# Performance work log

Hardware: AMD Instinct MI355X
Metric: run time of the kernel (lower is better)

## Reference

```python
import jax, jax.numpy as jnp
import numpy as np

S, B, D, L = 100, 2048, 128, 2  # seq_len, batch, dim_model, n_layers
LN_EPS = 1e-5


def _layer_norm(x, g, b):
    # x: [S, B, D]; normalize over last dim (nn.LayerNorm(dim))
    mu = jnp.mean(x, axis=-1, keepdims=True)
    var = jnp.mean(jnp.square(x - mu), axis=-1, keepdims=True)
    return (x - mu) * jax.lax.rsqrt(var + LN_EPS) * g + b


def _asb(x, cw, cwh, thr):
    # Adaptive_Spectral_Block. x: [S, B, D] -> permute to [B, N, C]
    xb = jnp.transpose(x, (1, 0, 2)).astype(jnp.float32)  # [B, N, C]
    N = xb.shape[1]
    x_fft = jnp.fft.rfft(xb, axis=1, norm='ortho')  # [B, F, C] complex, F = N//2+1
    w = jax.lax.complex(cw[:, 0], cw[:, 1])          # [C]
    x_weighted = x_fft * w
    # adaptive high-frequency mask
    energy = jnp.sum(jnp.square(jnp.abs(x_fft)), axis=-1)  # [B, F]
    F = energy.shape[1]
    # torch.median returns the LOWER of the two middle values -> k-th smallest, k=(F-1)//2
    median = jnp.sort(energy, axis=1)[:, (F - 1) // 2][:, None]  # [B, 1]
    norm_e = energy / (median + 1e-6)
    threshold = jnp.quantile(norm_e, thr)  # global scalar quantile (linear interp, as torch)
    mask = (norm_e < threshold)[..., None].astype(x_fft.real.dtype)  # [B, F, 1]
    wh = jax.lax.complex(cwh[:, 0], cwh[:, 1])       # [C]
    x_weighted = x_weighted + (x_fft * mask) * wh
    out = jnp.fft.irfft(x_weighted, n=N, axis=1, norm='ortho')  # [B, N, C]
    return jnp.transpose(out, (1, 0, 2)).astype(x.dtype)  # back to [S, B, D]


def setup_inputs() -> dict:
    key = jax.random.key(0)
    k0, k1, k2, k3 = jax.random.split(key, 4)
    return {
        'x': jax.random.normal(k0, (S, B, D), dtype=jnp.float32),
        'complex_weight': jax.random.normal(k1, (L, D, 2), dtype=jnp.float32) * 0.02,
        'complex_weight_high': jax.random.normal(k2, (L, D, 2), dtype=jnp.float32) * 0.02,
        'threshold_param': jax.random.uniform(k3, (L,), dtype=jnp.float32) * 0.5,
        'gamma': jnp.ones((L, D), dtype=jnp.float32),
        'beta': jnp.zeros((L, D), dtype=jnp.float32),
    }


def reference(x, complex_weight, complex_weight_high, threshold_param, gamma, beta):
    # Encoder.forward: nlayers x (x = x + ASB(LayerNorm(x)))
    for i in range(L):
        h = _layer_norm(x, gamma[i], beta[i])
        x = x + _asb(h, complex_weight[i], complex_weight_high[i], threshold_param[i])
    return x
```

## Files before the change

kernel.cpp:

```cpp
#include <hip/hip_runtime.h>
#include <math.h>

#define SEQ    100
#define BATCH  2048
#define DIM    128
#define NF     51
#define NLAYER 2
#define MTOT   (BATCH * NF)
#define BD     (BATCH * DIM)

typedef __attribute__((ext_vector_type(8))) short bf16x8;
typedef __attribute__((ext_vector_type(4))) float f32x4v;

__device__ __forceinline__ unsigned short f2bf(float f) {
    unsigned u = __float_as_uint(f);
    return (unsigned short)((u + 0x7FFFu + ((u >> 16) & 1u)) >> 16);
}

__global__ void k_tables(unsigned short* __restrict__ imgF,
                         unsigned short* __restrict__ imgI) {
    const int i = blockIdx.x * 256 + threadIdx.x;
    const float W = 6.28318530717958647692f / 100.f;
    if (i < 2 * 64 * 128) {
        const int p = i >> 13, k = (i >> 7) & 63, n = i & 127;
        float v = 0.f;
        if (k < NF && n < SEQ) {
            float s, c; sincosf((float)((k * n) % 100) * W, &s, &c);
            v = 0.1f * (p ? -s : c);
        }
        imgF[i] = f2bf(v);
    }
    if (i < 2 * 128 * 64) {
        const int p = i >> 13, n = (i >> 6) & 127, k = i & 63;
        float v = 0.f;
        if (k < NF && n < SEQ) {
            float s, c; sincosf((float)((k * n) % 100) * W, &s, &c);
            const float a = (k == 0 || k == 50) ? 0.1f : 0.2f;
            v = p ? -a * s : a * c;
        }
        imgI[i] = f2bf(v);
    }
}

__device__ __forceinline__ void ln_stage(const float* __restrict__ x,
                                         const float* __restrict__ gamma,
                                         const float* __restrict__ beta,
                                         unsigned short* hT, int b, int t)
{
    const int lane = t & 63, wv = t >> 6;
    const int c0 = lane * 2;
    const float2 gv = *(const float2*)&gamma[c0];
    const float2 bv = *(const float2*)&beta[c0];

    #pragma unroll
    for (int slot = 0; slot < 4; ++slot) {
        const int chunk = slot * 4 + wv;
        const int n0 = chunk * 8;
        float2 v[8];
        #pragma unroll
        for (int j = 0; j < 8; ++j)
            if (n0 + j < SEQ)
                v[j] = *(const float2*)&x[(size_t)(n0 + j) * BD + (size_t)b * DIM + c0];
        unsigned we[4], wo[4];
        #pragma unroll
        for (int j = 0; j < 8; ++j) {
            unsigned short he = 0, ho = 0;
            if (n0 + j < SEQ) {
                float s  = v[j].x + v[j].y;
                float s2 = fmaf(v[j].x, v[j].x, v[j].y * v[j].y);
                #pragma unroll
                for (int off = 1; off < 64; off <<= 1) {
                    s  += __shfl_xor(s,  off, 64);
                    s2 += __shfl_xor(s2, off, 64);
                }
                const float mu   = s * (1.f / 128.f);
                const float rstd = rsqrtf(s2 * (1.f / 128.f) - mu * mu + 1e-5f);
                he = f2bf(fmaf((v[j].x - mu) * rstd, gv.x, bv.x));
                ho = f2bf(fmaf((v[j].y - mu) * rstd, gv.y, bv.y));
            }
            if (j & 1) { we[j >> 1] |= (unsigned)he << 16; wo[j >> 1] |= (unsigned)ho << 16; }
            else       { we[j >> 1]  = he;                 wo[j >> 1]  = ho; }
        }
        const int sw = (chunk ^ (lane & 7)) << 3;
        int4 ve; ve.x = (int)we[0]; ve.y = (int)we[1]; ve.z = (int)we[2]; ve.w = (int)we[3];
        int4 vo; vo.x = (int)wo[0]; vo.y = (int)wo[1]; vo.z = (int)wo[2]; vo.w = (int)wo[3];
        *(int4*)&hT[(c0    ) * 128 + sw] = ve;
        *(int4*)&hT[(c0 + 1) * 128 + sw] = vo;
    }
}

__global__ __launch_bounds__(256, 4) void k_fwd(
    const float* __restrict__ x,
    const float* __restrict__ gamma, const float* __restrict__ beta,
    const unsigned short* __restrict__ imgF,
    float* __restrict__ normE)
{
    __shared__ __align__(16) unsigned short hT[128 * 128];
    __shared__ float epart[64][4];
    __shared__ float energy_s[64];
    __shared__ float med_s;

    const int b = blockIdx.x, t = threadIdx.x;
    const int lane = t & 63, wv = t >> 6, g4 = lane >> 4, cc = lane & 15;

    ln_stage(x, gamma, beta, hT, b, t);
    __syncthreads();

    bf16x8 Bf[2][4];
    #pragma unroll
    for (int ct = 0; ct < 2; ++ct) {
        const int c = wv * 32 + ct * 16 + cc;
        #pragma unroll
        for (int ks = 0; ks < 4; ++ks)
            Bf[ct][ks] = *(const bf16x8*)&hT[c * 128 + (((ks * 4 + g4) ^ (cc >> 1)) << 3)];
    }

    #pragma unroll
    for (int mt = 0; mt < 4; ++mt) {
        const int kr = mt * 16 + cc;
        f32x4v aR[2], aI[2];
        aR[0] = aR[1] = aI[0] = aI[1] = (f32x4v){0.f, 0.f, 0.f, 0.f};
        #pragma unroll
        for (int ks = 0; ks < 4; ++ks) {
            const int e0 = kr * 128 + ks * 32 + g4 * 8;
            const bf16x8 A0 = *(const bf16x8*)&imgF[e0];
            const bf16x8 A1 = *(const bf16x8*)&imgF[8192 + e0];
            #pragma unroll
            for (int ct = 0; ct < 2; ++ct) {
                aR[ct] = __builtin_amdgcn_mfma_f32_16x16x32_bf16(A0, Bf[ct][ks], aR[ct], 0, 0, 0);
                aI[ct] = __builtin_amdgcn_mfma_f32_16x16x32_bf16(A1, Bf[ct][ks], aI[ct], 0, 0, 0);
            }
        }
        #pragma unroll
        for (int reg = 0; reg < 4; ++reg) {
            float e = aR[0][reg] * aR[0][reg] + aI[0][reg] * aI[0][reg]
                    + aR[1][reg] * aR[1][reg] + aI[1][reg] * aI[1][reg];
            e += __shfl_xor(e, 1, 64); e += __shfl_xor(e, 2, 64);
            e += __shfl_xor(e, 4, 64); e += __shfl_xor(e, 8, 64);
            if (cc == 0) epart[mt * 16 + g4 * 4 + reg][wv] = e;
        }
    }
    __syncthreads();
    if (t < 64) energy_s[t] = epart[t][0] + epart[t][1] + epart[t][2] + epart[t][3];
    __syncthreads();
    if (t < NF) {
        const float e = energy_s[t];
        int cnt = 0;
        for (int j = 0; j < NF; ++j) {
            const float ej = energy_s[j];
            cnt += (ej < e || (ej == e && j < t)) ? 1 : 0;
        }
        if (cnt == (NF - 1) / 2) med_s = e;
    }
    __syncthreads();
    if (t < NF) normE[b * NF + t] = energy_s[t] / (med_s + 1e-6f);
}

__global__ void k_hist0(const float* __restrict__ normE,
                        unsigned* __restrict__ hist)
{
    __shared__ unsigned lh[2048];
    for (int i = threadIdx.x; i < 2048; i += 256) lh[i] = 0;
    __syncthreads();
    for (int i = blockIdx.x * 256 + threadIdx.x; i < MTOT; i += gridDim.x * 256)
        atomicAdd(&lh[__float_as_uint(normE[i]) >> 21], 1u);
    __syncthreads();
    for (int i = threadIdx.x; i < 2048; i += 256) {
        const unsigned c = lh[i];
        if (c) atomicAdd(&hist[i], c);
    }
}

__global__ void k_sel(const float* __restrict__ normE,
                      unsigned* __restrict__ hist,
                      unsigned* __restrict__ sel,
                      unsigned* __restrict__ done,
                      const float* __restrict__ thrp,
                      const int layer, const int phase,
                      float* __restrict__ thresh)
{
    __shared__ unsigned lh[4096];
    __shared__ unsigned sp[2], sc[2];
    __shared__ unsigned ticket_s;
    __shared__ float vb[2];
    const int t = threadIdx.x;
    const float q = thrp[layer] * (float)(MTOT - 1);
    const unsigned r0 = (unsigned)floorf(q);

    if (phase == 1) {
        if (t < 128) {
            const int j = t >> 6, ln = t & 63;
            const unsigned rk = r0 + (unsigned)j;
            unsigned sum = 0;
            for (int i = 0; i < 32; ++i) sum += hist[ln * 32 + i];
            unsigned pre = sum;
            #pragma unroll
            for (int off = 1; off < 64; off <<= 1) {
                const unsigned tt = __shfl_up(pre, off, 64);
                if (ln >= off) pre += tt;
            }
            const unsigned excl = pre - sum;
            if (rk >= excl && rk < excl + sum) {
                unsigned cum = excl;
                for (int i = 0; i < 32; ++i) {
                    const unsigned hc = hist[ln * 32 + i];
                    if (rk < cum + hc) { sp[j] = (unsigned)(ln * 32 + i) << 21; sc[j] = cum; break; }
                    cum += hc;
                }
            }
        }
    } else {
        if (t < 2) { sp[t] = sel[2 * t]; sc[t] = sel[2 * t + 1]; }
    }
    __syncthreads();
    const unsigned p0 = sp[0], p1 = sp[1];
    const int bins      = (phase == 1) ? 2048 : 1024;
    const int shift     = (phase == 1) ? 10 : 0;
    const unsigned hmsk = (phase == 1) ? 0xFFE00000u : 0xFFFFFC00u;
    const int region    = (phase == 1) ? 2048 : 6144;

    for (int i = t; i < 2 * bins; i += 256) lh[i] = 0;
    __syncthreads();
    for (int i = blockIdx.x * 256 + t; i < MTOT; i += gridDim.x * 256) {
        const unsigned v = __float_as_uint(normE[i]);
        const unsigned bin = (v >> shift) & (unsigned)(bins - 1);
        if ((v & hmsk) == p0) atomicAdd(&lh[bin], 1u);
        if ((v & hmsk) == p1) atomicAdd(&lh[bins + bin], 1u);
    }
    __syncthreads();
    for (int i = t; i < 2 * bins; i += 256) {
        const unsigned c = lh[i];
        if (c) atomicAdd(&hist[region + i], c);
    }
    __threadfence();
    if (t == 0) ticket_s = atomicAdd(&done[(layer << 1) + (phase - 1)], 1u);
    __syncthreads();
    if (ticket_s != (unsigned)(gridDim.x - 1)) return;
    __threadfence();

    if (t < 128) {
        const int j = t >> 6, ln = t & 63;
        const unsigned rk  = r0 + (unsigned)j;
        const unsigned rem = rk - sc[j];
        const unsigned* H  = hist + region + j * bins;
        const int per = bins / 64;
        unsigned sum = 0;
        for (int i = 0; i < per; ++i)
            sum += __hip_atomic_load(&H[ln * per + i], __ATOMIC_RELAXED, __HIP_MEMORY_SCOPE_AGENT);
        unsigned pre = sum;
        #pragma unroll
        for (int off = 1; off < 64; off <<= 1) {
            const unsigned tt = __shfl_up(pre, off, 64);
            if (ln >= off) pre += tt;
        }
        const unsigned excl = pre - sum;
        if (rem >= excl && rem < excl + sum) {
            unsigned cum = excl;
            for (int i = 0; i < per; ++i) {
                const unsigned hc = __hip_atomic_load(&H[ln * per + i],
                                        __ATOMIC_RELAXED, __HIP_MEMORY_SCOPE_AGENT);
                if (rem < cum + hc) {
                    const unsigned bin = (unsigned)(ln * per + i);
                    if (phase == 1) { sel[2 * j] = sp[j] | (bin << 10); sel[2 * j + 1] = sc[j] + cum; }
                    else            vb[j] = __uint_as_float(sp[j] | bin);
                    break;
                }
                cum += hc;
            }
        }
    }
    __syncthreads();
    if (phase == 1) { for (int i = t; i < 6144; i += 256) hist[i] = 0u; }
    else            { for (int i = t; i < 2048; i += 256) hist[6144 + i] = 0u; }
    if (t == 0) {
        done[(layer << 1) + (phase - 1)] = 0u;
        if (phase == 2) {
            const float frac = q - floorf(q);
            thresh[0] = vb[0] * (1.f - frac) + vb[1] * frac;
        }
    }
}

__global__ __launch_bounds__(256, 4) void k_asb(
    const float* __restrict__ x,
    const float* __restrict__ gamma, const float* __restrict__ beta,
    const float* __restrict__ cw, const float* __restrict__ cwh,
    const unsigned short* __restrict__ imgF,
    const unsigned short* __restrict__ imgI,
    const float* __restrict__ normE, const float* __restrict__ thresh,
    float* __restrict__ out)
{
    __shared__ __align__(16) unsigned short hT[128 * 128];
    __shared__ float mask_s[64];

    const int b = blockIdx.x, t = threadIdx.x;
    const int lane = t & 63, wv = t >> 6, g4 = lane >> 4, cc = lane & 15;

    if (t < 64) mask_s[t] = (t < NF && normE[b * NF + t] < thresh[0]) ? 1.f : 0.f;
    ln_stage(x, gamma, beta, hT, b, t);
    __syncthreads();

    bf16x8 Bf[2][4];
    #pragma unroll
    for (int ct = 0; ct < 2; ++ct) {
        const int c = wv * 32 + ct * 16 + cc;
        #pragma unroll
        for (int ks = 0; ks < 4; ++ks)
            Bf[ct][ks] = *(const bf16x8*)&hT[c * 128 + (((ks * 4 + g4) ^ (cc >> 1)) << 3)];
    }

    float fwr[2], fwi[2], fhr[2], fhi[2];
    #pragma unroll
    for (int ct = 0; ct < 2; ++ct) {
        const int c = wv * 32 + ct * 16 + cc;
        const float2 w2 = *(const float2*)&cw[2 * c];
        const float2 h2 = *(const float2*)&cwh[2 * c];
        fwr[ct] = w2.x; fwi[ct] = w2.y; fhr[ct] = h2.x; fhi[ct] = h2.y;
    }

    #pragma unroll
    for (int mt = 0; mt < 4; ++mt) {
        const int kr = mt * 16 + cc;
        f32x4v aR[2], aI[2];
        aR[0] = aR[1] = aI[0] = aI[1] = (f32x4v){0.f, 0.f, 0.f, 0.f};
        #pragma unroll
        for (int ks = 0; ks < 4; ++ks) {
            const int e0 = kr * 128 + ks * 32 + g4 * 8;
            const bf16x8 A0 = *(const bf16x8*)&imgF[e0];
            const bf16x8 A1 = *(const bf16x8*)&imgF[8192 + e0];
            #pragma unroll
            for (int ct = 0; ct < 2; ++ct) {
                aR[ct] = __builtin_amdgcn_mfma_f32_16x16x32_bf16(A0, Bf[ct][ks], aR[ct], 0, 0, 0);
                aI[ct] = __builtin_amdgcn_mfma_f32_16x16x32_bf16(A1, Bf[ct][ks], aI[ct], 0, 0, 0);
            }
        }
        #pragma unroll
        for (int ct = 0; ct < 2; ++ct) {
            const int c = wv * 32 + ct * 16 + cc;
            unsigned wr[2], wi[2];
            #pragma unroll
            for (int reg = 0; reg < 4; ++reg) {
                const float m   = mask_s[mt * 16 + g4 * 4 + reg];
                const float fre = fmaf(m, fhr[ct], fwr[ct]);
                const float fim = fmaf(m, fhi[ct], fwi[ct]);
                const float xr = aR[ct][reg], xi = aI[ct][reg];
                const unsigned short yr = f2bf(xr * fre - xi * fim);
                const unsigned short yi = f2bf(xr * fim + xi * fre);
                if (reg & 1) { wr[reg >> 1] |= (unsigned)yr << 16; wi[reg >> 1] |= (unsigned)yi << 16; }
                else         { wr[reg >> 1]  = yr;                 wi[reg >> 1]  = yi; }
            }
            const int chY = mt * 2 + (g4 >> 1);
            const int eb  = c * 128 + ((chY ^ (cc >> 1)) << 3) + (g4 & 1) * 4;
            int2 vr; vr.x = (int)wr[0]; vr.y = (int)wr[1];
            int2 vi; vi.x = (int)wi[0]; vi.y = (int)wi[1];
            *(int2*)&hT[eb]      = vr;
            *(int2*)&hT[eb + 64] = vi;
        }
    }

    bf16x8 Yr[2][2], Yi[2][2];
    #pragma unroll
    for (int ct = 0; ct < 2; ++ct) {
        const int c = wv * 32 + ct * 16 + cc;
        #pragma unroll
        for (int kb = 0; kb < 2; ++kb) {
            const int sw = (((kb * 4 + g4) ^ (cc >> 1)) << 3);
            Yr[ct][kb] = *(const bf16x8*)&hT[c * 128 + sw];
            Yi[ct][kb] = *(const bf16x8*)&hT[c * 128 + 64 + sw];
        }
    }

    #pragma unroll
    for (int mt = 0; mt < 7; ++mt) {
        const int nr = mt * 16 + cc;
        f32x4v o[2];
        o[0] = o[1] = (f32x4v){0.f, 0.f, 0.f, 0.f};
        #pragma unroll
        for (int kb = 0; kb < 2; ++kb) {
            const int e0 = nr * 64 + kb * 32 + g4 * 8;
            const bf16x8 A0 = *(const bf16x8*)&imgI[e0];
            const bf16x8 A1 = *(const bf16x8*)&imgI[8192 + e0];
            #pragma unroll
            for (int ct = 0; ct < 2; ++ct) {
                o[ct] = __builtin_amdgcn_mfma_f32_16x16x32_bf16(A0, Yr[ct][kb], o[ct], 0, 0, 0);
                o[ct] = __builtin_amdgcn_mfma_f32_16x16x32_bf16(A1, Yi[ct][kb], o[ct], 0, 0, 0);
            }
        }
        #pragma unroll
        for (int ct = 0; ct < 2; ++ct) {
            const int c = wv * 32 + ct * 16 + cc;
            #pragma unroll
            for (int reg = 0; reg < 4; ++reg) {
                const int n = mt * 16 + g4 * 4 + reg;
                if (n < SEQ) {
                    const size_t idx = (size_t)n * BD + (size_t)b * DIM + c;
                    out[idx] = x[idx] + o[ct][reg];
                }
            }
        }
    }
}

extern "C" void kernel_launch(void* const* d_in, const int* in_sizes, int n_in,
                              void* d_out, int out_size, void* d_ws, size_t ws_size,
                              hipStream_t stream)
{
    (void)in_sizes; (void)n_in; (void)out_size; (void)ws_size;
    const float* x    = (const float*)d_in[0];
    const float* cw   = (const float*)d_in[1];
    const float* cwh  = (const float*)d_in[2];
    const float* thrp = (const float*)d_in[3];
    const float* gam  = (const float*)d_in[4];
    const float* bet  = (const float*)d_in[5];
    float* out = (float*)d_out;

    char* ws = (char*)d_ws;
    unsigned short* imgF = (unsigned short*)(ws);
    unsigned short* imgI = (unsigned short*)(ws + 32768);
    float* normE   = (float*)(ws + 65536);
    unsigned* hist = (unsigned*)(ws + 483328);
    unsigned* done = (unsigned*)(ws + 516096);
    unsigned* sel  = (unsigned*)(ws + 516160);
    float* thresh  = (float*)(ws + 516224);

    k_tables<<<64, 256, 0, stream>>>(imgF, imgI);
    hipMemsetAsync(hist, 0, 32768 + 64, stream);

    for (int l = 0; l < NLAYER; ++l) {
        const float* xi = (l == 0) ? x : out;
        k_fwd<<<BATCH, 256, 0, stream>>>(xi, gam + l * DIM, bet + l * DIM,
                                         imgF, normE);
        k_hist0<<<96, 256, 0, stream>>>(normE, hist);
        k_sel<<<96, 256, 0, stream>>>(normE, hist, sel, done, thrp, l, 1, thresh);
        k_sel<<<96, 256, 0, stream>>>(normE, hist, sel, done, thrp, l, 2, thresh);
        k_asb<<<BATCH, 256, 0, stream>>>(xi, gam + l * DIM, bet + l * DIM,
                                         cw + l * DIM * 2, cwh + l * DIM * 2,
                                         imgF, imgI, normE, thresh, out);
    }
}
```

Baseline: 423.7 us.

## Store forward spectrum in workspace and skip LayerNorm+DFT recompute in ASB kernel

k_fwd now writes the bf16 forward-DFT spectrum (real and imaginary, per batch and channel) into a 64 MB workspace buffer. k_asb reads that buffer and applies the weight and mask directly, so it no longer repeats the LayerNorm and forward DFT matmuls. The LN stage is also inlined, with all x loads issued before any reduction to raise memory-level parallelism. The trade is extra global write and read traffic of about 64 MB each per layer, and a larger workspace, in return for removing redundant compute and x reads in the second kernel.

```diff
diff --git a/kernel.cpp b/kernel.cpp
--- a/kernel.cpp
+++ b/kernel.cpp
@@ -8,6 +8,7 @@
 #define NLAYER 2
 #define MTOT   (BATCH * NF)
 #define BD     (BATCH * DIM)
+#define XSTR   16384
 
 typedef __attribute__((ext_vector_type(8))) short bf16x8;
 typedef __attribute__((ext_vector_type(4))) float f32x4v;
@@ -15,6 +16,9 @@
 __device__ __forceinline__ unsigned short f2bf(float f) {
     unsigned u = __float_as_uint(f);
     return (unsigned short)((u + 0x7FFFu + ((u >> 16) & 1u)) >> 16);
+}
+__device__ __forceinline__ float bf2f(unsigned short u) {
+    return __uint_as_float((unsigned)u << 16);
 }
 
 __global__ void k_tables(unsigned short* __restrict__ imgF,
@@ -42,57 +46,11 @@
     }
 }
 
-__device__ __forceinline__ void ln_stage(const float* __restrict__ x,
-                                         const float* __restrict__ gamma,
-                                         const float* __restrict__ beta,
-                                         unsigned short* hT, int b, int t)
-{
-    const int lane = t & 63, wv = t >> 6;
-    const int c0 = lane * 2;
-    const float2 gv = *(const float2*)&gamma[c0];
-    const float2 bv = *(const float2*)&beta[c0];
-
-    #pragma unroll
-    for (int slot = 0; slot < 4; ++slot) {
-        const int chunk = slot * 4 + wv;
-        const int n0 = chunk * 8;
-        float2 v[8];
-        #pragma unroll
-        for (int j = 0; j < 8; ++j)
-            if (n0 + j < SEQ)
-                v[j] = *(const float2*)&x[(size_t)(n0 + j) * BD + (size_t)b * DIM + c0];
-        unsigned we[4], wo[4];
-        #pragma unroll
-        for (int j = 0; j < 8; ++j) {
-            unsigned short he = 0, ho = 0;
-            if (n0 + j < SEQ) {
-                float s  = v[j].x + v[j].y;
-                float s2 = fmaf(v[j].x, v[j].x, v[j].y * v[j].y);
-                #pragma unroll
-                for (int off = 1; off < 64; off <<= 1) {
-                    s  += __shfl_xor(s,  off, 64);
-                    s2 += __shfl_xor(s2, off, 64);
-                }
-                const float mu   = s * (1.f / 128.f);
-                const float rstd = rsqrtf(s2 * (1.f / 128.f) - mu * mu + 1e-5f);
-                he = f2bf(fmaf((v[j].x - mu) * rstd, gv.x, bv.x));
-                ho = f2bf(fmaf((v[j].y - mu) * rstd, gv.y, bv.y));
-            }
-            if (j & 1) { we[j >> 1] |= (unsigned)he << 16; wo[j >> 1] |= (unsigned)ho << 16; }
-            else       { we[j >> 1]  = he;                 wo[j >> 1]  = ho; }
-        }
-        const int sw = (chunk ^ (lane & 7)) << 3;
-        int4 ve; ve.x = (int)we[0]; ve.y = (int)we[1]; ve.z = (int)we[2]; ve.w = (int)we[3];
-        int4 vo; vo.x = (int)wo[0]; vo.y = (int)wo[1]; vo.z = (int)wo[2]; vo.w = (int)wo[3];
-        *(int4*)&hT[(c0    ) * 128 + sw] = ve;
-        *(int4*)&hT[(c0 + 1) * 128 + sw] = vo;
-    }
-}
-
 __global__ __launch_bounds__(256, 4) void k_fwd(
     const float* __restrict__ x,
     const float* __restrict__ gamma, const float* __restrict__ beta,
     const unsigned short* __restrict__ imgF,
+    unsigned short* __restrict__ Xg,
     float* __restrict__ normE)
 {
     __shared__ __align__(16) unsigned short hT[128 * 128];
@@ -103,7 +61,50 @@
     const int b = blockIdx.x, t = threadIdx.x;
     const int lane = t & 63, wv = t >> 6, g4 = lane >> 4, cc = lane & 15;
 
-    ln_stage(x, gamma, beta, hT, b, t);
+    {
+        const int c0 = lane * 2;
+        const float2 gv = *(const float2*)&gamma[c0];
+        const float2 bv = *(const float2*)&beta[c0];
+        float2 v[4][8];
+        #pragma unroll
+        for (int slot = 0; slot < 4; ++slot) {
+            const int n0 = (slot * 4 + wv) * 8;
+            #pragma unroll
+            for (int j = 0; j < 8; ++j)
+                if (n0 + j < SEQ)
+                    v[slot][j] = *(const float2*)&x[(size_t)(n0 + j) * BD + (size_t)b * DIM + c0];
+        }
+        #pragma unroll
+        for (int slot = 0; slot < 4; ++slot) {
+            const int chunk = slot * 4 + wv;
+            const int n0 = chunk * 8;
+            unsigned we[4], wo[4];
+            #pragma unroll
+            for (int j = 0; j < 8; ++j) {
+                unsigned short he = 0, ho = 0;
+                if (n0 + j < SEQ) {
+                    float s  = v[slot][j].x + v[slot][j].y;
+                    float s2 = fmaf(v[slot][j].x, v[slot][j].x, v[slot][j].y * v[slot][j].y);
+                    #pragma unroll
+                    for (int off = 1; off < 64; off <<= 1) {
+                        s  += __shfl_xor(s,  off, 64);
+                        s2 += __shfl_xor(s2, off, 64);
+                    }
+                    const float mu   = s * (1.f / 128.f);
+                    const float rstd = rsqrtf(s2 * (1.f / 128.f) - mu * mu + 1e-5f);
+                    he = f2bf(fmaf((v[slot][j].x - mu) * rstd, gv.x, bv.x));
+                    ho = f2bf(fmaf((v[slot][j].y - mu) * rstd, gv.y, bv.y));
+                }
+                if (j & 1) { we[j >> 1] |= (unsigned)he << 16; wo[j >> 1] |= (unsigned)ho << 16; }
+                else       { we[j >> 1]  = he;                 wo[j >> 1]  = ho; }
+            }
+            const int sw = (chunk ^ (lane & 7)) << 3;
+            int4 ve; ve.x = (int)we[0]; ve.y = (int)we[1]; ve.z = (int)we[2]; ve.w = (int)we[3];
+            int4 vo; vo.x = (int)wo[0]; vo.y = (int)wo[1]; vo.z = (int)wo[2]; vo.w = (int)wo[3];
+            *(int4*)&hT[(c0    ) * 128 + sw] = ve;
+            *(int4*)&hT[(c0 + 1) * 128 + sw] = vo;
+        }
+    }
     __syncthreads();
 
     bf16x8 Bf[2][4];
@@ -138,6 +139,19 @@
             e += __shfl_xor(e, 1, 64); e += __shfl_xor(e, 2, 64);
             e += __shfl_xor(e, 4, 64); e += __shfl_xor(e, 8, 64);
             if (cc == 0) epart[mt * 16 + g4 * 4 + reg][wv] = e;
+        }
+        #pragma unroll
+        for (int ct = 0; ct < 2; ++ct) {
+            const int c = wv * 32 + ct * 16 + cc;
+            unsigned short* Xb = Xg + (size_t)b * XSTR + (size_t)c * 128;
+            const int k0 = mt * 16 + g4 * 4;
+            uint2 pr, pi;
+            pr.x = (unsigned)f2bf(aR[ct][0]) | ((unsigned)f2bf(aR[ct][1]) << 16);
+            pr.y = (unsigned)f2bf(aR[ct][2]) | ((unsigned)f2bf(aR[ct][3]) << 16);
+            pi.x = (unsigned)f2bf(aI[ct][0]) | ((unsigned)f2bf(aI[ct][1]) << 16);
+            pi.y = (unsigned)f2bf(aI[ct][2]) | ((unsigned)f2bf(aI[ct][3]) << 16);
+            *(uint2*)&Xb[k0]      = pr;
+            *(uint2*)&Xb[64 + k0] = pi;
         }
     }
     __syncthreads();
@@ -283,90 +297,43 @@
 
 __global__ __launch_bounds__(256, 4) void k_asb(
     const float* __restrict__ x,
-    const float* __restrict__ gamma, const float* __restrict__ beta,
     const float* __restrict__ cw, const float* __restrict__ cwh,
-    const unsigned short* __restrict__ imgF,
+    const unsigned short* __restrict__ Xg,
     const unsigned short* __restrict__ imgI,
     const float* __restrict__ normE, const float* __restrict__ thresh,
     float* __restrict__ out)
 {
-    __shared__ __align__(16) unsigned short hT[128 * 128];
     __shared__ float mask_s[64];
 
     const int b = blockIdx.x, t = threadIdx.x;
     const int lane = t & 63, wv = t >> 6, g4 = lane >> 4, cc = lane & 15;
 
     if (t < 64) mask_s[t] = (t < NF && normE[b * NF + t] < thresh[0]) ? 1.f : 0.f;
-    ln_stage(x, gamma, beta, hT, b, t);
-    __syncthreads();
-
-    bf16x8 Bf[2][4];
-    #pragma unroll
-    for (int ct = 0; ct < 2; ++ct) {
-        const int c = wv * 32 + ct * 16 + cc;
-        #pragma unroll
-        for (int ks = 0; ks < 4; ++ks)
-            Bf[ct][ks] = *(const bf16x8*)&hT[c * 128 + (((ks * 4 + g4) ^ (cc >> 1)) << 3)];
-    }
-
-    float fwr[2], fwi[2], fhr[2], fhi[2];
-    #pragma unroll
-    for (int ct = 0; ct < 2; ++ct) {
-        const int c = wv * 32 + ct * 16 + cc;
-        const float2 w2 = *(const float2*)&cw[2 * c];
-        const float2 h2 = *(const float2*)&cwh[2 * c];
-        fwr[ct] = w2.x; fwi[ct] = w2.y; fhr[ct] = h2.x; fhi[ct] = h2.y;
-    }
-
-    #pragma unroll
-    for (int mt = 0; mt < 4; ++mt) {
-        const int kr = mt * 16 + cc;
-        f32x4v aR[2], aI[2];
-        aR[0] = aR[1] = aI[0] = aI[1] = (f32x4v){0.f, 0.f, 0.f, 0.f};
-        #pragma unroll
-        for (int ks = 0; ks < 4; ++ks) {
-            const int e0 = kr * 128 + ks * 32 + g4 * 8;
-            const bf16x8 A0 = *(const bf16x8*)&imgF[e0];
-            const bf16x8 A1 = *(const bf16x8*)&imgF[8192 + e0];
-            #pragma unroll
-            for (int ct = 0; ct < 2; ++ct) {
-                aR[ct] = __builtin_amdgcn_mfma_f32_16x16x32_bf16(A0, Bf[ct][ks], aR[ct], 0, 0, 0);
-                aI[ct] = __builtin_amdgcn_mfma_f32_16x16x32_bf16(A1, Bf[ct][ks], aI[ct], 0, 0, 0);
-            }
-        }
-        #pragma unroll
-        for (int ct = 0; ct < 2; ++ct) {
-            const int c = wv * 32 + ct * 16 + cc;
-            unsigned wr[2], wi[2];
-            #pragma unroll
-            for (int reg = 0; reg < 4; ++reg) {
-                const float m   = mask_s[mt * 16 + g4 * 4 + reg];
-                const float fre = fmaf(m, fhr[ct], fwr[ct]);
-                const float fim = fmaf(m, fhi[ct], fwi[ct]);
-                const float xr = aR[ct][reg], xi = aI[ct][reg];
-                const unsigned short yr = f2bf(xr * fre - xi * fim);
-                const unsigned short yi = f2bf(xr * fim + xi * fre);
-                if (reg & 1) { wr[reg >> 1] |= (unsigned)yr << 16; wi[reg >> 1] |= (unsigned)yi << 16; }
-                else         { wr[reg >> 1]  = yr;                 wi[reg >> 1]  = yi; }
-            }
-            const int chY = mt * 2 + (g4 >> 1);
-            const int eb  = c * 128 + ((chY ^ (cc >> 1)) << 3) + (g4 & 1) * 4;
-            int2 vr; vr.x = (int)wr[0]; vr.y = (int)wr[1];
-            int2 vi; vi.x = (int)wi[0]; vi.y = (int)wi[1];
-            *(int2*)&hT[eb]      = vr;
-            *(int2*)&hT[eb + 64] = vi;
-        }
-    }
+    __syncthreads();
 
     bf16x8 Yr[2][2], Yi[2][2];
     #pragma unroll
     for (int ct = 0; ct < 2; ++ct) {
         const int c = wv * 32 + ct * 16 + cc;
+        const unsigned short* Xb = Xg + (size_t)b * XSTR + (size_t)c * 128;
+        const float2 w2 = *(const float2*)&cw[2 * c];
+        const float2 h2 = *(const float2*)&cwh[2 * c];
         #pragma unroll
         for (int kb = 0; kb < 2; ++kb) {
-            const int sw = (((kb * 4 + g4) ^ (cc >> 1)) << 3);
-            Yr[ct][kb] = *(const bf16x8*)&hT[c * 128 + sw];
-            Yi[ct][kb] = *(const bf16x8*)&hT[c * 128 + 64 + sw];
+            const bf16x8 xr = *(const bf16x8*)&Xb[kb * 32 + g4 * 8];
+            const bf16x8 xi = *(const bf16x8*)&Xb[64 + kb * 32 + g4 * 8];
+            bf16x8 yr, yi;
+            #pragma unroll
+            for (int j = 0; j < 8; ++j) {
+                const float m   = mask_s[kb * 32 + g4 * 8 + j];
+                const float fre = fmaf(m, h2.x, w2.x);
+                const float fim = fmaf(m, h2.y, w2.y);
+                const float fxr = bf2f((unsigned short)xr[j]);
+                const float fxi = bf2f((unsigned short)xi[j]);
+                yr[j] = (short)f2bf(fxr * fre - fxi * fim);
+                yi[j] = (short)f2bf(fxr * fim + fxi * fre);
+            }
+            Yr[ct][kb] = yr; Yi[ct][kb] = yi;
         }
     }
 
@@ -417,11 +384,12 @@
     char* ws = (char*)d_ws;
     unsigned short* imgF = (unsigned short*)(ws);
     unsigned short* imgI = (unsigned short*)(ws + 32768);
-    float* normE   = (float*)(ws + 65536);
-    unsigned* hist = (unsigned*)(ws + 483328);
-    unsigned* done = (unsigned*)(ws + 516096);
-    unsigned* sel  = (unsigned*)(ws + 516160);
-    float* thresh  = (float*)(ws + 516224);
+    unsigned short* Xg   = (unsigned short*)(ws + 65536);
+    float* normE   = (float*)(ws + 65536 + 67108864);
+    unsigned* hist = (unsigned*)(ws + 65536 + 67108864 + 417792);
+    unsigned* done = (unsigned*)(ws + 65536 + 67108864 + 417792 + 32768);
+    unsigned* sel  = (unsigned*)(ws + 65536 + 67108864 + 417792 + 32768 + 64);
+    float* thresh  = (float*)(ws + 65536 + 67108864 + 417792 + 32768 + 128);
 
     k_tables<<<64, 256, 0, stream>>>(imgF, imgI);
     hipMemsetAsync(hist, 0, 32768 + 64, stream);
@@ -429,12 +397,11 @@
     for (int l = 0; l < NLAYER; ++l) {
         const float* xi = (l == 0) ? x : out;
         k_fwd<<<BATCH, 256, 0, stream>>>(xi, gam + l * DIM, bet + l * DIM,
-                                         imgF, normE);
+                                         imgF, Xg, normE);
         k_hist0<<<96, 256, 0, stream>>>(normE, hist);
         k_sel<<<96, 256, 0, stream>>>(normE, hist, sel, done, thrp, l, 1, thresh);
         k_sel<<<96, 256, 0, stream>>>(normE, hist, sel, done, thrp, l, 2, thresh);
-        k_asb<<<BATCH, 256, 0, stream>>>(xi, gam + l * DIM, bet + l * DIM,
-                                         cw + l * DIM * 2, cwh + l * DIM * 2,
-                                         imgF, imgI, normE, thresh, out);
-    }
-}
+        k_asb<<<BATCH, 256, 0, stream>>>(xi, cw + l * DIM * 2, cwh + l * DIM * 2,
+                                         Xg, imgI, normE, thresh, out);
+    }
+}
```

Result: faster. 351.6 us (-17.0%).
